# Performance work log

Measured on AMD Instinct MI355X. Metric: run time of the kernel, lower is better.

## Reference

```python
import jax, jax.numpy as jnp
import numpy as np

VOCAB, D, L, H, B, S = 10000, 512, 6, 8, 32, 384
DK = D // H
DFF = 4 * D
EPS = 1e-5


def setup_inputs() -> dict:
    key = jax.random.key(0)
    ks = jax.random.split(key, 24)
    sc = 0.02
    emb = jax.random.normal(ks[0], (VOCAB, D), jnp.float32) * sc
    emb = emb.at[0].set(0.0)  # padding_idx=0
    inp = {
        'input_id': jax.random.randint(ks[1], (B, S), 0, VOCAB),
        'intensity': jax.random.uniform(ks[2], (B, 1, S), jnp.float32),
        'emb': emb,
        'iw': jax.random.normal(ks[3], (1, D), jnp.float32) * sc,
        'ib': jnp.zeros((D,), jnp.float32),
        'Wq': jax.random.normal(ks[4], (L, D, D), jnp.float32) * sc,
        'bq': jnp.zeros((L, D), jnp.float32),
        'Wk': jax.random.normal(ks[5], (L, D, D), jnp.float32) * sc,
        'bk': jnp.zeros((L, D), jnp.float32),
        'Wv': jax.random.normal(ks[6], (L, D, D), jnp.float32) * sc,
        'bv': jnp.zeros((L, D), jnp.float32),
        'Wo': jax.random.normal(ks[7], (L, D, D), jnp.float32) * sc,
        'bo': jnp.zeros((L, D), jnp.float32),
        'ln1w': jnp.ones((L, D), jnp.float32),
        'ln1b': jnp.zeros((L, D), jnp.float32),
        'ln2w': jnp.ones((L, D), jnp.float32),
        'ln2b': jnp.zeros((L, D), jnp.float32),
        'W1': jax.random.normal(ks[8], (L, D, DFF), jnp.float32) * sc,
        'b1': jnp.zeros((L, DFF), jnp.float32),
        'W2': jax.random.normal(ks[9], (L, DFF, D), jnp.float32) * sc,
        'b2': jnp.zeros((L, D), jnp.float32),
    }
    return inp


def _ln(x, w, b):
    m = jnp.mean(x, axis=-1, keepdims=True)
    v = jnp.mean((x - m) ** 2, axis=-1, keepdims=True)
    return (x - m) / jnp.sqrt(v + EPS) * w + b


def _block(x, pad_mask, Wq, bq, Wk, bk, Wv, bv, Wo, bo, ln1w, ln1b, ln2w, ln2b, W1, b1, W2, b2):
    b, s, d = x.shape
    h = _ln(x, ln1w, ln1b)
    q = (h @ Wq + bq).reshape(b, s, H, DK).transpose(0, 2, 1, 3)  # [B,H,S,DK]
    k = (h @ Wk + bk).reshape(b, s, H, DK).transpose(0, 2, 1, 3)
    v = (h @ Wv + bv).reshape(b, s, H, DK).transpose(0, 2, 1, 3)
    scores = jnp.einsum('bhqd,bhkd->bhqk', q, k) / jnp.sqrt(jnp.float32(DK))
    scores = jnp.where(pad_mask, -1e9, scores)  # mask keys at pad positions
    p = jax.nn.softmax(scores, axis=-1)
    attn = jnp.einsum('bhqk,bhkd->bhqd', p, v)
    attn = attn.transpose(0, 2, 1, 3).reshape(b, s, d)
    x = x + (attn @ Wo + bo)
    h2 = _ln(x, ln2w, ln2b)
    ffn = jax.nn.gelu(h2 @ W1 + b1, approximate=False) @ W2 + b2
    return x + ffn


def reference(input_id, intensity, emb, iw, ib, Wq, bq, Wk, bk, Wv, bv, Wo, bo,
              ln1w, ln1b, ln2w, ln2b, W1, b1, W2, b2):
    # predict() path of MSBERT (deterministic; training forward adds random masking)
    inten = jnp.swapaxes(intensity, 1, 2) @ iw + ib          # [B,S,D]
    x = emb[input_id] + inten                                 # token emb + intensity proj
    pad_mask = (input_id == 0)[:, None, None, :]              # [B,1,1,S] broadcast over queries
    for i in range(L):
        x = _block(x, pad_mask, Wq[i], bq[i], Wk[i], bk[i], Wv[i], bv[i], Wo[i], bo[i],
                   ln1w[i], ln1b[i], ln2w[i], ln2b[i], W1[i], b1[i], W2[i], b2[i])
    pool = jnp.matmul(intensity, x) / jnp.float32(intensity.shape[1])  # [B,1,D]
    return pool
```

## Files before the change

### kernel.cpp

```cpp
#include <hip/hip_runtime.h>
#include <math.h>

#define VOCAB 10000
#define D 512
#define L 6
#define H 8
#define B 32
#define S 384
#define DK 64
#define DFF 2048
#define TOK (B * S)
#define TD ((size_t)TOK * D)

typedef unsigned short u16;
using bf16x8 = __attribute__((ext_vector_type(8))) short;
using f32x4  = __attribute__((ext_vector_type(4))) float;
using u16x4  = __attribute__((ext_vector_type(4))) unsigned short;

__device__ u16   g_x[TD];
__device__ u16   g_h[TD];
__device__ u16   g_q[TD];
__device__ u16   g_k[TD];
__device__ u16   g_vt[TD];
__device__ u16   g_ffn[(size_t)TOK * DFF];
__device__ u16   g_qkvT[(size_t)L * 3 * D * D];
__device__ u16   g_woT[(size_t)L * D * D];
__device__ u16   g_w1T[(size_t)L * DFF * D];
__device__ u16   g_w2T[(size_t)L * D * DFF];
__device__ float g_bqkv[L * 3 * D];
__device__ float g_pool[B * 6 * D];

__device__ __forceinline__ u16 f2bf(float f) {
  unsigned int u = __builtin_bit_cast(unsigned int, f);
  u = (u + 0x7fffu + ((u >> 16) & 1u)) >> 16;
  return (u16)u;
}
__device__ __forceinline__ float bf2f(u16 v) {
  unsigned int u = ((unsigned int)v) << 16;
  return __builtin_bit_cast(float, u);
}

__device__ __forceinline__ void gld16(const void* g, void* l) {
  __builtin_amdgcn_global_load_lds(
      (const __attribute__((address_space(1))) unsigned int*)g,
      (__attribute__((address_space(3))) unsigned int*)l, 16, 0, 0);
}

__global__ __launch_bounds__(256) void embed_kernel(
    const int* __restrict__ ids, const float* __restrict__ inten,
    const float* __restrict__ emb, const float* __restrict__ iw,
    const float* __restrict__ ib, u16* __restrict__ x) {
  int tok = blockIdx.x;
  int t = threadIdx.x;
  int id = ids[tok];
  float it = inten[tok];
  const float* er = emb + (size_t)id * D;
  u16* xr = x + (size_t)tok * D;
  xr[t]       = f2bf(er[t] + it * iw[t] + ib[t]);
  xr[t + 256] = f2bf(er[t + 256] + it * iw[t + 256] + ib[t + 256]);
}

__global__ __launch_bounds__(256) void ln_kernel(
    const u16* __restrict__ x, const float* __restrict__ w,
    const float* __restrict__ b, u16* __restrict__ out) {
  int tok = blockIdx.x * 4 + (threadIdx.x >> 6);
  int lane = threadIdx.x & 63;
  const u16* xr = x + (size_t)tok * D + lane * 8;
  bf16x8 v8 = *(const bf16x8*)xr;
  float v[8];
  float s = 0.f, ss = 0.f;
  #pragma unroll
  for (int i = 0; i < 8; ++i) {
    v[i] = bf2f((u16)v8[i]);
    s += v[i];
    ss += v[i] * v[i];
  }
  #pragma unroll
  for (int o = 1; o < 64; o <<= 1) {
    s += __shfl_xor(s, o);
    ss += __shfl_xor(ss, o);
  }
  float mean = s * (1.0f / (float)D);
  float var = ss * (1.0f / (float)D) - mean * mean;
  float rstd = rsqrtf(var + 1e-5f);
  float4 w0 = *(const float4*)(w + lane * 8);
  float4 w1 = *(const float4*)(w + lane * 8 + 4);
  float4 b0 = *(const float4*)(b + lane * 8);
  float4 b1 = *(const float4*)(b + lane * 8 + 4);
  float wv[8] = {w0.x, w0.y, w0.z, w0.w, w1.x, w1.y, w1.z, w1.w};
  float bv[8] = {b0.x, b0.y, b0.z, b0.w, b1.x, b1.y, b1.z, b1.w};
  bf16x8 o8;
  #pragma unroll
  for (int i = 0; i < 8; ++i)
    o8[i] = (short)f2bf((v[i] - mean) * rstd * wv[i] + bv[i]);
  *(bf16x8*)(out + (size_t)tok * D + lane * 8) = o8;
}

__global__ __launch_bounds__(256) void transpose_cvt(
    const float* __restrict__ src, u16* __restrict__ dst,
    int K, int N, size_t sstride, size_t dstride) {
  __shared__ float tile[32][33];
  int n0 = blockIdx.x * 32, k0 = blockIdx.y * 32, l = blockIdx.z;
  src += (size_t)l * sstride;
  dst += (size_t)l * dstride;
  int tx = threadIdx.x & 31, ty = threadIdx.x >> 5;
  #pragma unroll
  for (int i = 0; i < 32; i += 8)
    tile[ty + i][tx] = src[(size_t)(k0 + ty + i) * N + n0 + tx];
  __syncthreads();
  #pragma unroll
  for (int i = 0; i < 32; i += 8)
    dst[(size_t)(n0 + ty + i) * K + k0 + tx] = f2bf(tile[tx][ty + i]);
}

__global__ __launch_bounds__(256) void transpose_qkvo(
    const float* __restrict__ Wq, const float* __restrict__ Wk,
    const float* __restrict__ Wv, const float* __restrict__ Wo,
    u16* __restrict__ qkvT, u16* __restrict__ woT) {
  __shared__ float tile[32][33];
  int z = blockIdx.z;
  int l = z >> 2, which = z & 3;
  const float* src = (which == 0 ? Wq : which == 1 ? Wk : which == 2 ? Wv : Wo)
                     + (size_t)l * D * D;
  u16* dst = (which < 3) ? (qkvT + (size_t)l * 3 * D * D + (size_t)which * D * D)
                         : (woT + (size_t)l * D * D);
  int n0 = blockIdx.x * 32, k0 = blockIdx.y * 32;
  int tx = threadIdx.x & 31, ty = threadIdx.x >> 5;
  #pragma unroll
  for (int i = 0; i < 32; i += 8)
    tile[ty + i][tx] = src[(size_t)(k0 + ty + i) * D + n0 + tx];
  __syncthreads();
  #pragma unroll
  for (int i = 0; i < 32; i += 8)
    dst[(size_t)(n0 + ty + i) * D + k0 + tx] = f2bf(tile[tx][ty + i]);
}

__global__ __launch_bounds__(256) void concat_bias(
    const float* __restrict__ bq, const float* __restrict__ bk,
    const float* __restrict__ bv, float* __restrict__ dst) {
  int i = blockIdx.x * 256 + threadIdx.x;
  int l = i / 1536, c = i % 1536;
  float v = (c < 512) ? bq[l * 512 + c]
          : (c < 1024) ? bk[l * 512 + c - 512]
                       : bv[l * 512 + c - 1024];
  dst[i] = v;
}

template <int EPI>
__global__ __launch_bounds__(256) void mfma_gemm(
    const u16* __restrict__ A, const u16* __restrict__ Bt,
    const float* __restrict__ bias,
    u16* __restrict__ Oq, u16* __restrict__ Ok, u16* __restrict__ Ovt,
    int M, int N, int K) {
  __shared__ u16 As[2][128 * 32];
  __shared__ u16 Bs[2][128 * 32];
  int t = threadIdx.x;
  int lane = t & 63, w = t >> 6;
  int wr = w >> 1, wc = w & 1;

  int gm = gridDim.y, gn = gridDim.x;
  int wgid = blockIdx.y * gn + blockIdx.x;
  int xcd = wgid & 7;
  int c = wgid >> 3;
  int rpx = gm >> 3;
  int cg = c / gn;
  int bm = (xcd * rpx + cg) * 128;
  int bn = (c - cg * gn) * 128;

  int l15 = lane & 15, l4 = lane >> 4;

  int gswu = ((t & 3) ^ ((t >> 3) & 3)) * 8;
  const u16* a0 = A + (size_t)(bm + (t >> 2)) * K + gswu;
  const u16* a1 = A + (size_t)(bm + 64 + (t >> 2)) * K + gswu;
  const u16* b0 = Bt + (size_t)(bn + (t >> 2)) * K + gswu;
  const u16* b1 = Bt + (size_t)(bn + 64 + (t >> 2)) * K + gswu;
  unsigned off0 = (unsigned)(t & 192) * 16u;
  unsigned off1 = off0 + 256u * 16u;
  int rxu = (l4 ^ ((l15 >> 1) & 3)) * 8;

  f32x4 acc[4][4];
  #pragma unroll
  for (int mi = 0; mi < 4; ++mi)
    #pragma unroll
    for (int nj = 0; nj < 4; ++nj)
      acc[mi][nj] = f32x4{0.f, 0.f, 0.f, 0.f};

  int nt = K >> 5;

#define STAGE_T(ti, bi) do { int k0s = (ti) * 32;            \
    gld16(a0 + k0s, (char*)As[bi] + off0);                   \
    gld16(a1 + k0s, (char*)As[bi] + off1);                   \
    gld16(b0 + k0s, (char*)Bs[bi] + off0);                   \
    gld16(b1 + k0s, (char*)Bs[bi] + off1); } while (0)

  STAGE_T(0, 0);
  STAGE_T(1, 1);

  for (int tt = 0; tt < nt; ++tt) {
    if (tt < nt - 1) asm volatile("s_waitcnt vmcnt(4)" ::: "memory");
    else             asm volatile("s_waitcnt vmcnt(0)" ::: "memory");
    __builtin_amdgcn_s_barrier();
    __builtin_amdgcn_sched_barrier(0);
    const u16* Asb = As[tt & 1];
    const u16* Bsb = Bs[tt & 1];
    bf16x8 af[4], bfr[4];
    #pragma unroll
    for (int mi = 0; mi < 4; ++mi)
      af[mi] = *(const bf16x8*)(Asb + (wr * 64 + mi * 16 + l15) * 32 + rxu);
    #pragma unroll
    for (int nj = 0; nj < 4; ++nj)
      bfr[nj] = *(const bf16x8*)(Bsb + (wc * 64 + nj * 16 + l15) * 32 + rxu);
    #pragma unroll
    for (int mi = 0; mi < 4; ++mi)
      #pragma unroll
      for (int nj = 0; nj < 4; ++nj)
        acc[mi][nj] = __builtin_amdgcn_mfma_f32_16x16x32_bf16(af[mi], bfr[nj], acc[mi][nj], 0, 0, 0);
    __builtin_amdgcn_sched_barrier(0);
    __builtin_amdgcn_s_barrier();
    if (tt + 2 < nt) STAGE_T(tt + 2, tt & 1);
  }
#undef STAGE_T

  int row00 = bm + wr * 64, col0 = bn + wc * 64;
  #pragma unroll
  for (int mi = 0; mi < 4; ++mi) {
    int rowb = row00 + mi * 16 + l4 * 4;
    #pragma unroll
    for (int nj = 0; nj < 4; ++nj) {
      int col = col0 + nj * 16 + l15;
      float bcol = bias[col];
      if (EPI == 0) {
        if (col < 512) {
          #pragma unroll
          for (int r = 0; r < 4; ++r)
            Oq[(size_t)(rowb + r) * D + col] = f2bf(acc[mi][nj][r] + bcol);
        } else if (col < 1024) {
          #pragma unroll
          for (int r = 0; r < 4; ++r)
            Ok[(size_t)(rowb + r) * D + (col - 512)] = f2bf(acc[mi][nj][r] + bcol);
        } else {
          int cv = col - 1024;
          int hh = cv >> 6, dk = cv & 63;
          int bb = rowb / S, ss = rowb - bb * S;
          u16x4 pk;
          #pragma unroll
          for (int r = 0; r < 4; ++r) pk[r] = f2bf(acc[mi][nj][r] + bcol);
          *(u16x4*)(Ovt + ((size_t)(bb * H + hh) * DK + dk) * S + ss) = pk;
        }
      } else {
        #pragma unroll
        for (int r = 0; r < 4; ++r) {
          float v = acc[mi][nj][r] + bcol;
          v = 0.5f * v * (1.0f + erff(v * 0.70710678118654752f));
          Oq[(size_t)(rowb + r) * N + col] = f2bf(v);
        }
      }
    }
  }
}

__global__ __launch_bounds__(256) void gemm64(
    const u16* __restrict__ A, const u16* __restrict__ Bt,
    const float* __restrict__ bias, u16* __restrict__ Cres,
    int M, int N, int K) {
  __shared__ u16 As[2][64 * 32];
  __shared__ u16 Bs[2][128 * 32];
  int t = threadIdx.x;
  int lane = t & 63, w = t >> 6;
  int wr = w >> 1, wc = w & 1;

  int gm = gridDim.y, gn = gridDim.x;
  int wgid = blockIdx.y * gn + blockIdx.x;
  int xcd = wgid & 7;
  int c = wgid >> 3;
  int rpx = gm >> 3;
  int cg = c / gn;
  int bm = (xcd * rpx + cg) * 64;
  int bn = (c - cg * gn) * 128;

  int l15 = lane & 15, l4 = lane >> 4;

  int arow = t >> 2, ag = t & 3;
  int aswu = (ag ^ ((arow >> 1) & 3)) * 8;
  const u16* a0 = A + (size_t)(bm + arow) * K + aswu;
  const u16* b0 = Bt + (size_t)(bn + arow) * K + aswu;
  const u16* b1 = Bt + (size_t)(bn + 64 + arow) * K + aswu;
  unsigned offA  = (unsigned)(w * 1024);
  unsigned offB0 = (unsigned)(w * 1024);
  unsigned offB1 = offB0 + 4096u;
  int rxu = (l4 ^ ((l15 >> 1) & 3)) * 8;

  f32x4 acc[2][4];
  #pragma unroll
  for (int mi = 0; mi < 2; ++mi)
    #pragma unroll
    for (int nj = 0; nj < 4; ++nj)
      acc[mi][nj] = f32x4{0.f, 0.f, 0.f, 0.f};

  int nt = K >> 5;

#define STG64(ti, bi) do { int k0s = (ti) * 32;              \
    gld16(a0 + k0s, (char*)As[bi] + offA);                   \
    gld16(b0 + k0s, (char*)Bs[bi] + offB0);                  \
    gld16(b1 + k0s, (char*)Bs[bi] + offB1); } while (0)

  STG64(0, 0);
  STG64(1, 1);

  for (int tt = 0; tt < nt; ++tt) {
    if (tt < nt - 1) asm volatile("s_waitcnt vmcnt(3)" ::: "memory");
    else             asm volatile("s_waitcnt vmcnt(0)" ::: "memory");
    __builtin_amdgcn_s_barrier();
    __builtin_amdgcn_sched_barrier(0);
    const u16* Asb = As[tt & 1];
    const u16* Bsb = Bs[tt & 1];
    bf16x8 af[2], bfr[4];
    #pragma unroll
    for (int mi = 0; mi < 2; ++mi)
      af[mi] = *(const bf16x8*)(Asb + (wr * 32 + mi * 16 + l15) * 32 + rxu);
    #pragma unroll
    for (int nj = 0; nj < 4; ++nj)
      bfr[nj] = *(const bf16x8*)(Bsb + (wc * 64 + nj * 16 + l15) * 32 + rxu);
    #pragma unroll
    for (int mi = 0; mi < 2; ++mi)
      #pragma unroll
      for (int nj = 0; nj < 4; ++nj)
        acc[mi][nj] = __builtin_amdgcn_mfma_f32_16x16x32_bf16(af[mi], bfr[nj], acc[mi][nj], 0, 0, 0);
    __builtin_amdgcn_sched_barrier(0);
    __builtin_amdgcn_s_barrier();
    if (tt + 2 < nt) STG64(tt + 2, tt & 1);
  }
#undef STG64

  int row00 = bm + wr * 32, col0 = bn + wc * 64;
  #pragma unroll
  for (int mi = 0; mi < 2; ++mi) {
    int rowb = row00 + mi * 16 + l4 * 4;
    #pragma unroll
    for (int nj = 0; nj < 4; ++nj) {
      int col = col0 + nj * 16 + l15;
      float bcol = bias[col];
      #pragma unroll
      for (int r = 0; r < 4; ++r) {
        size_t ci = (size_t)(rowb + r) * N + col;
        Cres[ci] = f2bf(bf2f(Cres[ci]) + acc[mi][nj][r] + bcol);
      }
    }
  }
}

__global__ __launch_bounds__(256) void attn_mfma(
    const u16* __restrict__ q, const u16* __restrict__ k,
    const u16* __restrict__ vt, const int* __restrict__ ids,
    u16* __restrict__ out) {
  __shared__ u16 Ks[64][72];
  __shared__ u16 Vs[64][72];
  __shared__ u16 Ps[4][32][72];
  __shared__ float Msall[S];
  int t = threadIdx.x, lane = t & 63, w = t >> 6;
  int l15 = lane & 15, l4 = lane >> 4;
  int bh = blockIdx.x;
  int b = bh >> 3, hh = bh & 7;
  int q0 = blockIdx.y * 128 + w * 32;

  for (int i = t; i < S; i += 256)
    Msall[i] = (ids[b * S + i] == 0) ? -1e9f : 0.0f;

  bf16x8 qf[2][2];
  const u16* qbase = q + (size_t)(b * S + q0) * D + hh * DK;
  #pragma unroll
  for (int mi = 0; mi < 2; ++mi)
    #pragma unroll
    for (int ks = 0; ks < 2; ++ks)
      qf[mi][ks] = *(const bf16x8*)(qbase + (size_t)(mi * 16 + l15) * D + ks * 32 + l4 * 8);

  int rr0 = t >> 3, ch0 = t & 7;
  int rr1 = (256 + t) >> 3, ch1 = t & 7;
  const size_t kbase = (size_t)(b * S) * D + hh * DK;
  const size_t vbase = (size_t)(b * H + hh) * DK * S;

  bf16x8 kr0, kr1, vr0, vr1;
  kr0 = *(const bf16x8*)(k + kbase + (size_t)rr0 * D + ch0 * 8);
  kr1 = *(const bf16x8*)(k + kbase + (size_t)rr1 * D + ch1 * 8);
  vr0 = *(const bf16x8*)(vt + vbase + (size_t)rr0 * S + 0 + ch0 * 8);
  vr1 = *(const bf16x8*)(vt + vbase + (size_t)rr1 * S + 0 + ch1 * 8);
  *(bf16x8*)(&Ks[rr0][ch0 * 8]) = kr0;
  *(bf16x8*)(&Ks[rr1][ch1 * 8]) = kr1;
  *(bf16x8*)(&Vs[rr0][ch0 * 8]) = vr0;
  *(bf16x8*)(&Vs[rr1][ch1 * 8]) = vr1;
  __syncthreads();

  float m[8], lsum[8];
  f32x4 accO[2][4];
  #pragma unroll
  for (int i = 0; i < 8; ++i) { m[i] = -3e38f; lsum[i] = 0.f; }
  #pragma unroll
  for (int mi = 0; mi < 2; ++mi)
    #pragma unroll
    for (int nj = 0; nj < 4; ++nj)
      accO[mi][nj] = f32x4{0.f, 0.f, 0.f, 0.f};

  for (int kb = 0; kb < S; kb += 64) {
    bool more = (kb + 64) < S;
    if (more) {
      kr0 = *(const bf16x8*)(k + kbase + (size_t)(kb + 64 + rr0) * D + ch0 * 8);
      kr1 = *(const bf16x8*)(k + kbase + (size_t)(kb + 64 + rr1) * D + ch1 * 8);
      vr0 = *(const bf16x8*)(vt + vbase + (size_t)rr0 * S + kb + 64 + ch0 * 8);
      vr1 = *(const bf16x8*)(vt + vbase + (size_t)rr1 * S + kb + 64 + ch1 * 8);
    }

    f32x4 sc[2][4];
    #pragma unroll
    for (int mi = 0; mi < 2; ++mi)
      #pragma unroll
      for (int nj = 0; nj < 4; ++nj)
        sc[mi][nj] = f32x4{0.f, 0.f, 0.f, 0.f};
    __builtin_amdgcn_s_setprio(1);
    #pragma unroll
    for (int ks = 0; ks < 2; ++ks) {
      bf16x8 kf[4];
      #pragma unroll
      for (int nj = 0; nj < 4; ++nj)
        kf[nj] = *(const bf16x8*)(&Ks[nj * 16 + l15][ks * 32 + l4 * 8]);
      #pragma unroll
      for (int mi = 0; mi < 2; ++mi)
        #pragma unroll
        for (int nj = 0; nj < 4; ++nj)
          sc[mi][nj] = __builtin_amdgcn_mfma_f32_16x16x32_bf16(qf[mi][ks], kf[nj], sc[mi][nj], 0, 0, 0);
    }
    __builtin_amdgcn_s_setprio(0);
    #pragma unroll
    for (int mi = 0; mi < 2; ++mi)
      #pragma unroll
      for (int nj = 0; nj < 4; ++nj) {
        float mv = Msall[kb + nj * 16 + l15];
        #pragma unroll
        for (int r = 0; r < 4; ++r)
          sc[mi][nj][r] = sc[mi][nj][r] * 0.125f + mv;
      }
    #pragma unroll
    for (int mi = 0; mi < 2; ++mi)
      #pragma unroll
      for (int r = 0; r < 4; ++r) {
        int ridx = mi * 4 + r;
        float mx = sc[mi][0][r];
        #pragma unroll
        for (int nj = 1; nj < 4; ++nj) mx = fmaxf(mx, sc[mi][nj][r]);
        #pragma unroll
        for (int o = 1; o < 16; o <<= 1) mx = fmaxf(mx, __shfl_xor(mx, o));
        float mnew = fmaxf(m[ridx], mx);
        float scale = __expf(m[ridx] - mnew);
        float rs = 0.f;
        #pragma unroll
        for (int nj = 0; nj < 4; ++nj) {
          float p = __expf(sc[mi][nj][r] - mnew);
          sc[mi][nj][r] = p;
          rs += p;
        }
        #pragma unroll
        for (int o = 1; o < 16; o <<= 1) rs += __shfl_xor(rs, o);
        lsum[ridx] = lsum[ridx] * scale + rs;
        m[ridx] = mnew;
        #pragma unroll
        for (int nj = 0; nj < 4; ++nj) accO[mi][nj][r] *= scale;
      }
    #pragma unroll
    for (int mi = 0; mi < 2; ++mi)
      #pragma unroll
      for (int nj = 0; nj < 4; ++nj)
        #pragma unroll
        for (int r = 0; r < 4; ++r)
          Ps[w][mi * 16 + l4 * 4 + r][nj * 16 + l15] = f2bf(sc[mi][nj][r]);
    __builtin_amdgcn_s_setprio(1);
    #pragma unroll
    for (int ks2 = 0; ks2 < 2; ++ks2) {
      bf16x8 pf[2], vf[4];
      #pragma unroll
      for (int mi = 0; mi < 2; ++mi)
        pf[mi] = *(const bf16x8*)(&Ps[w][mi * 16 + l15][ks2 * 32 + l4 * 8]);
      #pragma unroll
      for (int nj = 0; nj < 4; ++nj)
        vf[nj] = *(const bf16x8*)(&Vs[nj * 16 + l15][ks2 * 32 + l4 * 8]);
      #pragma unroll
      for (int mi = 0; mi < 2; ++mi)
        #pragma unroll
        for (int nj = 0; nj < 4; ++nj)
          accO[mi][nj] = __builtin_amdgcn_mfma_f32_16x16x32_bf16(pf[mi], vf[nj], accO[mi][nj], 0, 0, 0);
    }
    __builtin_amdgcn_s_setprio(0);

    if (more) {
      __syncthreads();
      *(bf16x8*)(&Ks[rr0][ch0 * 8]) = kr0;
      *(bf16x8*)(&Ks[rr1][ch1 * 8]) = kr1;
      *(bf16x8*)(&Vs[rr0][ch0 * 8]) = vr0;
      *(bf16x8*)(&Vs[rr1][ch1 * 8]) = vr1;
      __syncthreads();
    }
  }

  #pragma unroll
  for (int mi = 0; mi < 2; ++mi)
    #pragma unroll
    for (int nj = 0; nj < 4; ++nj)
      #pragma unroll
      for (int r = 0; r < 4; ++r) {
        int row = b * S + q0 + mi * 16 + l4 * 4 + r;
        out[(size_t)row * D + hh * DK + nj * 16 + l15] =
            f2bf(accO[mi][nj][r] / lsum[mi * 4 + r]);
      }
}

__global__ __launch_bounds__(512) void pool_part(
    const u16* __restrict__ x, const float* __restrict__ inten,
    float* __restrict__ part) {
  int b = blockIdx.x, cchunk = blockIdx.y;
  int d = threadIdx.x;
  int s0 = cchunk * 64;
  float acc = 0.f;
  for (int s = s0; s < s0 + 64; ++s)
    acc += inten[b * S + s] * bf2f(x[((size_t)b * S + s) * D + d]);
  part[((size_t)b * 6 + cchunk) * D + d] = acc;
}
__global__ __launch_bounds__(512) void pool_reduce(
    const float* __restrict__ part, float* __restrict__ out) {
  int b = blockIdx.x, d = threadIdx.x;
  float acc = 0.f;
  #pragma unroll
  for (int c = 0; c < 6; ++c) acc += part[((size_t)b * 6 + c) * D + d];
  out[b * D + d] = acc;
}

extern "C" void kernel_launch(void* const* d_in, const int* in_sizes, int n_in,
                              void* d_out, int out_size, void* d_ws, size_t ws_size,
                              hipStream_t stream) {
  const int* input_id    = (const int*)d_in[0];
  const float* intensity = (const float*)d_in[1];
  const float* emb = (const float*)d_in[2];
  const float* iw  = (const float*)d_in[3];
  const float* ib  = (const float*)d_in[4];
  const float* Wq  = (const float*)d_in[5];
  const float* bq  = (const float*)d_in[6];
  const float* Wk  = (const float*)d_in[7];
  const float* bk  = (const float*)d_in[8];
  const float* Wv  = (const float*)d_in[9];
  const float* bv  = (const float*)d_in[10];
  const float* Wo  = (const float*)d_in[11];
  const float* bo  = (const float*)d_in[12];
  const float* ln1w = (const float*)d_in[13];
  const float* ln1b = (const float*)d_in[14];
  const float* ln2w = (const float*)d_in[15];
  const float* ln2b = (const float*)d_in[16];
  const float* W1  = (const float*)d_in[17];
  const float* b1  = (const float*)d_in[18];
  const float* W2  = (const float*)d_in[19];
  const float* b2  = (const float*)d_in[20];
  float* outp = (float*)d_out;

  float *bqkv, *poolp;
  u16 *x, *h, *q, *k, *vt, *ffn, *qkvT, *woT, *w1T, *w2T;
  { void* p; hipGetSymbolAddress(&p, HIP_SYMBOL(g_x));    x    = (u16*)p; }
  { void* p; hipGetSymbolAddress(&p, HIP_SYMBOL(g_h));    h    = (u16*)p; }
  { void* p; hipGetSymbolAddress(&p, HIP_SYMBOL(g_q));    q    = (u16*)p; }
  { void* p; hipGetSymbolAddress(&p, HIP_SYMBOL(g_k));    k    = (u16*)p; }
  { void* p; hipGetSymbolAddress(&p, HIP_SYMBOL(g_vt));   vt   = (u16*)p; }
  { void* p; hipGetSymbolAddress(&p, HIP_SYMBOL(g_ffn));  ffn  = (u16*)p; }
  { void* p; hipGetSymbolAddress(&p, HIP_SYMBOL(g_qkvT)); qkvT = (u16*)p; }
  { void* p; hipGetSymbolAddress(&p, HIP_SYMBOL(g_woT));  woT  = (u16*)p; }
  { void* p; hipGetSymbolAddress(&p, HIP_SYMBOL(g_w1T));  w1T  = (u16*)p; }
  { void* p; hipGetSymbolAddress(&p, HIP_SYMBOL(g_w2T));  w2T  = (u16*)p; }
  { void* p; hipGetSymbolAddress(&p, HIP_SYMBOL(g_bqkv)); bqkv = (float*)p; }
  { void* p; hipGetSymbolAddress(&p, HIP_SYMBOL(g_pool)); poolp = (float*)p; }

  dim3 t256(256);
  transpose_qkvo<<<dim3(16, 16, 4 * L), t256, 0, stream>>>(Wq, Wk, Wv, Wo, qkvT, woT);
  transpose_cvt<<<dim3(64, 16, L), t256, 0, stream>>>(W1, w1T, D, DFF, (size_t)D * DFF, (size_t)D * DFF);
  transpose_cvt<<<dim3(16, 64, L), t256, 0, stream>>>(W2, w2T, DFF, D, (size_t)DFF * D, (size_t)DFF * D);
  concat_bias<<<L * 3 * D / 256, t256, 0, stream>>>(bq, bk, bv, bqkv);

  embed_kernel<<<TOK, t256, 0, stream>>>(input_id, intensity, emb, iw, ib, x);

  for (int l = 0; l < L; ++l) {
    const u16* qkvT_l = qkvT + (size_t)l * 3 * D * D;
    const u16* woT_l  = woT + (size_t)l * D * D;
    const u16* w1T_l  = w1T + (size_t)l * D * DFF;
    const u16* w2T_l  = w2T + (size_t)l * DFF * D;

    ln_kernel<<<TOK / 4, t256, 0, stream>>>(x, ln1w + (size_t)l * D, ln1b + (size_t)l * D, h);
    mfma_gemm<0><<<dim3(12, 96), t256, 0, stream>>>(h, qkvT_l, bqkv + l * 3 * D,
                                                    q, k, vt, TOK, 3 * D, D);
    attn_mfma<<<dim3(B * H, S / 128), t256, 0, stream>>>(q, k, vt, input_id, h);
    gemm64<<<dim3(4, 192), t256, 0, stream>>>(h, woT_l, bo + (size_t)l * D,
                                              x, TOK, D, D);
    ln_kernel<<<TOK / 4, t256, 0, stream>>>(x, ln2w + (size_t)l * D, ln2b + (size_t)l * D, h);
    mfma_gemm<2><<<dim3(16, 96), t256, 0, stream>>>(h, w1T_l, b1 + (size_t)l * DFF,
                                                    ffn, nullptr, nullptr, TOK, DFF, D);
    gemm64<<<dim3(4, 192), t256, 0, stream>>>(ffn, w2T_l, b2 + (size_t)l * D,
                                              x, TOK, D, DFF);
  }

  pool_part<<<dim3(B, 6), dim3(512), 0, stream>>>(x, intensity, poolp);
  pool_reduce<<<B, dim3(512), 0, stream>>>(poolp, outp);
}
```

Before: 1.240 ms.

## Prepack weights into MFMA fragment layout and load B directly to registers

Weights are now converted once into a fragment-major bf16 layout that matches the MFMA B operand, so each wave can load its B fragments from global memory straight into registers instead of staging them through LDS. This cuts LDS traffic and LDS footprint in both GEMM kernels, keeps a two-deep register double buffer for B, and adjusts the vmcnt waits to match. Block order is also remapped so that consecutive workgroups on an XCD walk M first within the same N column, which should improve L2 reuse of B. The cost is more vector registers per thread and global B loads duplicated across the two row-waves, which now go through cache instead of shared memory.

```diff
diff --git a/kernel.cpp b/kernel.cpp
--- a/kernel.cpp
+++ b/kernel.cpp
@@ -23,10 +23,10 @@
 __device__ u16   g_k[TD];
 __device__ u16   g_vt[TD];
 __device__ u16   g_ffn[(size_t)TOK * DFF];
-__device__ u16   g_qkvT[(size_t)L * 3 * D * D];
-__device__ u16   g_woT[(size_t)L * D * D];
-__device__ u16   g_w1T[(size_t)L * DFF * D];
-__device__ u16   g_w2T[(size_t)L * D * DFF];
+__device__ u16   g_qkvB[(size_t)L * 3 * D * D];
+__device__ u16   g_woB[(size_t)L * D * D];
+__device__ u16   g_w1B[(size_t)L * DFF * D];
+__device__ u16   g_w2B[(size_t)L * D * DFF];
 __device__ float g_bqkv[L * 3 * D];
 __device__ float g_pool[B * 6 * D];
 
@@ -96,43 +96,23 @@
   *(bf16x8*)(out + (size_t)tok * D + lane * 8) = o8;
 }
 
-__global__ __launch_bounds__(256) void transpose_cvt(
-    const float* __restrict__ src, u16* __restrict__ dst,
-    int K, int N, size_t sstride, size_t dstride) {
-  __shared__ float tile[32][33];
-  int n0 = blockIdx.x * 32, k0 = blockIdx.y * 32, l = blockIdx.z;
-  src += (size_t)l * sstride;
-  dst += (size_t)l * dstride;
-  int tx = threadIdx.x & 31, ty = threadIdx.x >> 5;
-  #pragma unroll
-  for (int i = 0; i < 32; i += 8)
-    tile[ty + i][tx] = src[(size_t)(k0 + ty + i) * N + n0 + tx];
-  __syncthreads();
-  #pragma unroll
-  for (int i = 0; i < 32; i += 8)
-    dst[(size_t)(n0 + ty + i) * K + k0 + tx] = f2bf(tile[tx][ty + i]);
-}
-
-__global__ __launch_bounds__(256) void transpose_qkvo(
-    const float* __restrict__ Wq, const float* __restrict__ Wk,
-    const float* __restrict__ Wv, const float* __restrict__ Wo,
-    u16* __restrict__ qkvT, u16* __restrict__ woT) {
-  __shared__ float tile[32][33];
-  int z = blockIdx.z;
-  int l = z >> 2, which = z & 3;
-  const float* src = (which == 0 ? Wq : which == 1 ? Wk : which == 2 ? Wv : Wo)
-                     + (size_t)l * D * D;
-  u16* dst = (which < 3) ? (qkvT + (size_t)l * 3 * D * D + (size_t)which * D * D)
-                         : (woT + (size_t)l * D * D);
-  int n0 = blockIdx.x * 32, k0 = blockIdx.y * 32;
-  int tx = threadIdx.x & 31, ty = threadIdx.x >> 5;
-  #pragma unroll
-  for (int i = 0; i < 32; i += 8)
-    tile[ty + i][tx] = src[(size_t)(k0 + ty + i) * D + n0 + tx];
-  __syncthreads();
-  #pragma unroll
-  for (int i = 0; i < 32; i += 8)
-    dst[(size_t)(n0 + ty + i) * D + k0 + tx] = f2bf(tile[tx][ty + i]);
+__global__ __launch_bounds__(256) void prepack_b(
+    const float* __restrict__ W, u16* __restrict__ Bp,
+    int N, int K, size_t sstride, size_t dstride) {
+  int l = blockIdx.y;
+  W += (size_t)l * sstride;
+  Bp += (size_t)l * dstride;
+  int fi = blockIdx.x * 4 + (threadIdx.x >> 6);
+  int lane = threadIdx.x & 63;
+  int nfr = K >> 5;
+  int nb = fi / nfr, kb = fi - nb * nfr;
+  int col = nb * 16 + (lane & 15);
+  int row0 = kb * 32 + (lane >> 4) * 8;
+  bf16x8 o;
+  #pragma unroll
+  for (int j = 0; j < 8; ++j)
+    o[j] = (short)f2bf(W[(size_t)(row0 + j) * N + col]);
+  *(bf16x8*)(Bp + (size_t)fi * 512 + lane * 8) = o;
 }
 
 __global__ __launch_bounds__(256) void concat_bias(
@@ -148,36 +128,33 @@
 
 template <int EPI>
 __global__ __launch_bounds__(256) void mfma_gemm(
-    const u16* __restrict__ A, const u16* __restrict__ Bt,
+    const u16* __restrict__ A, const u16* __restrict__ Bp,
     const float* __restrict__ bias,
     u16* __restrict__ Oq, u16* __restrict__ Ok, u16* __restrict__ Ovt,
     int M, int N, int K) {
   __shared__ u16 As[2][128 * 32];
-  __shared__ u16 Bs[2][128 * 32];
   int t = threadIdx.x;
   int lane = t & 63, w = t >> 6;
   int wr = w >> 1, wc = w & 1;
+  int l15 = lane & 15, l4 = lane >> 4;
 
   int gm = gridDim.y, gn = gridDim.x;
   int wgid = blockIdx.y * gn + blockIdx.x;
-  int xcd = wgid & 7;
-  int c = wgid >> 3;
-  int rpx = gm >> 3;
-  int cg = c / gn;
-  int bm = (xcd * rpx + cg) * 128;
-  int bn = (c - cg * gn) * 128;
-
-  int l15 = lane & 15, l4 = lane >> 4;
+  int xcd = wgid & 7, c = wgid >> 3, rpx = gm >> 3;
+  int bni = c / rpx;
+  int bm = (xcd * rpx + (c - bni * rpx)) * 128;
+  int bn = bni * 128;
 
   int gswu = ((t & 3) ^ ((t >> 3) & 3)) * 8;
   const u16* a0 = A + (size_t)(bm + (t >> 2)) * K + gswu;
   const u16* a1 = A + (size_t)(bm + 64 + (t >> 2)) * K + gswu;
-  const u16* b0 = Bt + (size_t)(bn + (t >> 2)) * K + gswu;
-  const u16* b1 = Bt + (size_t)(bn + 64 + (t >> 2)) * K + gswu;
   unsigned off0 = (unsigned)(t & 192) * 16u;
   unsigned off1 = off0 + 256u * 16u;
   int rxu = (l4 ^ ((l15 >> 1) & 3)) * 8;
 
+  int nfr = K >> 5;
+  const u16* bpw = Bp + ((size_t)((bn >> 4) + wc * 4) * nfr) * 512 + lane * 8;
+
   f32x4 acc[4][4];
   #pragma unroll
   for (int mi = 0; mi < 4; ++mi)
@@ -185,41 +162,43 @@
     for (int nj = 0; nj < 4; ++nj)
       acc[mi][nj] = f32x4{0.f, 0.f, 0.f, 0.f};
 
-  int nt = K >> 5;
-
-#define STAGE_T(ti, bi) do { int k0s = (ti) * 32;            \
+  int nt = nfr;
+
+#define STAGE_A(ti, bi) do { int k0s = (ti) * 32;            \
     gld16(a0 + k0s, (char*)As[bi] + off0);                   \
-    gld16(a1 + k0s, (char*)As[bi] + off1);                   \
-    gld16(b0 + k0s, (char*)Bs[bi] + off0);                   \
-    gld16(b1 + k0s, (char*)Bs[bi] + off1); } while (0)
-
-  STAGE_T(0, 0);
-  STAGE_T(1, 1);
-
-  for (int tt = 0; tt < nt; ++tt) {
-    if (tt < nt - 1) asm volatile("s_waitcnt vmcnt(4)" ::: "memory");
-    else             asm volatile("s_waitcnt vmcnt(0)" ::: "memory");
-    __builtin_amdgcn_s_barrier();
-    __builtin_amdgcn_sched_barrier(0);
-    const u16* Asb = As[tt & 1];
-    const u16* Bsb = Bs[tt & 1];
-    bf16x8 af[4], bfr[4];
-    #pragma unroll
-    for (int mi = 0; mi < 4; ++mi)
-      af[mi] = *(const bf16x8*)(Asb + (wr * 64 + mi * 16 + l15) * 32 + rxu);
-    #pragma unroll
-    for (int nj = 0; nj < 4; ++nj)
-      bfr[nj] = *(const bf16x8*)(Bsb + (wc * 64 + nj * 16 + l15) * 32 + rxu);
-    #pragma unroll
-    for (int mi = 0; mi < 4; ++mi)
-      #pragma unroll
-      for (int nj = 0; nj < 4; ++nj)
-        acc[mi][nj] = __builtin_amdgcn_mfma_f32_16x16x32_bf16(af[mi], bfr[nj], acc[mi][nj], 0, 0, 0);
-    __builtin_amdgcn_sched_barrier(0);
-    __builtin_amdgcn_s_barrier();
-    if (tt + 2 < nt) STAGE_T(tt + 2, tt & 1);
-  }
-#undef STAGE_T
+    gld16(a1 + k0s, (char*)As[bi] + off1); } while (0)
+#define LOADB(ti, breg) do {                                 \
+    _Pragma("unroll") for (int nj = 0; nj < 4; ++nj)         \
+      breg[nj] = *(const bf16x8*)(bpw + ((size_t)nj * nfr + (ti)) * 512); } while (0)
+
+  bf16x8 brA[4], brB[4];
+  STAGE_A(0, 0); LOADB(0, brA);
+  STAGE_A(1, 1); LOADB(1, brB);
+
+#define GSTEP(tt, breg) do {                                             \
+    if ((tt) < nt - 1) asm volatile("s_waitcnt vmcnt(6)" ::: "memory");  \
+    else               asm volatile("s_waitcnt vmcnt(0)" ::: "memory");  \
+    __builtin_amdgcn_s_barrier();                                        \
+    __builtin_amdgcn_sched_barrier(0);                                   \
+    const u16* Asb = As[(tt) & 1];                                       \
+    bf16x8 af[4];                                                        \
+    _Pragma("unroll") for (int mi = 0; mi < 4; ++mi)                     \
+      af[mi] = *(const bf16x8*)(Asb + (wr * 64 + mi * 16 + l15) * 32 + rxu); \
+    _Pragma("unroll") for (int mi = 0; mi < 4; ++mi)                     \
+      _Pragma("unroll") for (int nj = 0; nj < 4; ++nj)                   \
+        acc[mi][nj] = __builtin_amdgcn_mfma_f32_16x16x32_bf16(af[mi], breg[nj], acc[mi][nj], 0, 0, 0); \
+    __builtin_amdgcn_sched_barrier(0);                                   \
+    __builtin_amdgcn_s_barrier();                                        \
+    if ((tt) + 2 < nt) { STAGE_A((tt) + 2, (tt) & 1); LOADB((tt) + 2, breg); } \
+  } while (0)
+
+  for (int tt = 0; tt < nt; tt += 2) {
+    GSTEP(tt, brA);
+    GSTEP(tt + 1, brB);
+  }
+#undef GSTEP
+#undef LOADB
+#undef STAGE_A
 
   int row00 = bm + wr * 64, col0 = bn + wc * 64;
   #pragma unroll
@@ -260,35 +239,31 @@
 }
 
 __global__ __launch_bounds__(256) void gemm64(
-    const u16* __restrict__ A, const u16* __restrict__ Bt,
+    const u16* __restrict__ A, const u16* __restrict__ Bp,
     const float* __restrict__ bias, u16* __restrict__ Cres,
     int M, int N, int K) {
   __shared__ u16 As[2][64 * 32];
-  __shared__ u16 Bs[2][128 * 32];
   int t = threadIdx.x;
   int lane = t & 63, w = t >> 6;
   int wr = w >> 1, wc = w & 1;
 
   int gm = gridDim.y, gn = gridDim.x;
   int wgid = blockIdx.y * gn + blockIdx.x;
-  int xcd = wgid & 7;
-  int c = wgid >> 3;
-  int rpx = gm >> 3;
-  int cg = c / gn;
-  int bm = (xcd * rpx + cg) * 64;
-  int bn = (c - cg * gn) * 128;
+  int xcd = wgid & 7, c = wgid >> 3, rpx = gm >> 3;
+  int bni = c / rpx;
+  int bm = (xcd * rpx + (c - bni * rpx)) * 64;
+  int bn = bni * 128;
 
   int l15 = lane & 15, l4 = lane >> 4;
 
   int arow = t >> 2, ag = t & 3;
   int aswu = (ag ^ ((arow >> 1) & 3)) * 8;
   const u16* a0 = A + (size_t)(bm + arow) * K + aswu;
-  const u16* b0 = Bt + (size_t)(bn + arow) * K + aswu;
-  const u16* b1 = Bt + (size_t)(bn + 64 + arow) * K + aswu;
-  unsigned offA  = (unsigned)(w * 1024);
-  unsigned offB0 = (unsigned)(w * 1024);
-  unsigned offB1 = offB0 + 4096u;
+  unsigned offA = (unsigned)(w * 1024);
   int rxu = (l4 ^ ((l15 >> 1) & 3)) * 8;
+
+  int nfr = K >> 5;
+  const u16* bpw = Bp + ((size_t)((bn >> 4) + wc * 4) * nfr) * 512 + lane * 8;
 
   f32x4 acc[2][4];
   #pragma unroll
@@ -297,40 +272,42 @@
     for (int nj = 0; nj < 4; ++nj)
       acc[mi][nj] = f32x4{0.f, 0.f, 0.f, 0.f};
 
-  int nt = K >> 5;
-
-#define STG64(ti, bi) do { int k0s = (ti) * 32;              \
-    gld16(a0 + k0s, (char*)As[bi] + offA);                   \
-    gld16(b0 + k0s, (char*)Bs[bi] + offB0);                  \
-    gld16(b1 + k0s, (char*)Bs[bi] + offB1); } while (0)
-
-  STG64(0, 0);
-  STG64(1, 1);
-
-  for (int tt = 0; tt < nt; ++tt) {
-    if (tt < nt - 1) asm volatile("s_waitcnt vmcnt(3)" ::: "memory");
-    else             asm volatile("s_waitcnt vmcnt(0)" ::: "memory");
-    __builtin_amdgcn_s_barrier();
-    __builtin_amdgcn_sched_barrier(0);
-    const u16* Asb = As[tt & 1];
-    const u16* Bsb = Bs[tt & 1];
-    bf16x8 af[2], bfr[4];
-    #pragma unroll
-    for (int mi = 0; mi < 2; ++mi)
-      af[mi] = *(const bf16x8*)(Asb + (wr * 32 + mi * 16 + l15) * 32 + rxu);
-    #pragma unroll
-    for (int nj = 0; nj < 4; ++nj)
-      bfr[nj] = *(const bf16x8*)(Bsb + (wc * 64 + nj * 16 + l15) * 32 + rxu);
-    #pragma unroll
-    for (int mi = 0; mi < 2; ++mi)
-      #pragma unroll
-      for (int nj = 0; nj < 4; ++nj)
-        acc[mi][nj] = __builtin_amdgcn_mfma_f32_16x16x32_bf16(af[mi], bfr[nj], acc[mi][nj], 0, 0, 0);
-    __builtin_amdgcn_sched_barrier(0);
-    __builtin_amdgcn_s_barrier();
-    if (tt + 2 < nt) STG64(tt + 2, tt & 1);
-  }
-#undef STG64
+  int nt = nfr;
+
+#define STAGE_A(ti, bi) \
+    gld16(a0 + (ti) * 32, (char*)As[bi] + offA)
+#define LOADB(ti, breg) do {                                 \
+    _Pragma("unroll") for (int nj = 0; nj < 4; ++nj)         \
+      breg[nj] = *(const bf16x8*)(bpw + ((size_t)nj * nfr + (ti)) * 512); } while (0)
+
+  bf16x8 brA[4], brB[4];
+  STAGE_A(0, 0); LOADB(0, brA);
+  STAGE_A(1, 1); LOADB(1, brB);
+
+#define GSTEP(tt, breg) do {                                             \
+    if ((tt) < nt - 1) asm volatile("s_waitcnt vmcnt(5)" ::: "memory");  \
+    else               asm volatile("s_waitcnt vmcnt(0)" ::: "memory");  \
+    __builtin_amdgcn_s_barrier();                                        \
+    __builtin_amdgcn_sched_barrier(0);                                   \
+    const u16* Asb = As[(tt) & 1];                                       \
+    bf16x8 af[2];                                                        \
+    _Pragma("unroll") for (int mi = 0; mi < 2; ++mi)                     \
+      af[mi] = *(const bf16x8*)(Asb + (wr * 32 + mi * 16 + l15) * 32 + rxu); \
+    _Pragma("unroll") for (int mi = 0; mi < 2; ++mi)                     \
+      _Pragma("unroll") for (int nj = 0; nj < 4; ++nj)                   \
+        acc[mi][nj] = __builtin_amdgcn_mfma_f32_16x16x32_bf16(af[mi], breg[nj], acc[mi][nj], 0, 0, 0); \
+    __builtin_amdgcn_sched_barrier(0);                                   \
+    __builtin_amdgcn_s_barrier();                                        \
+    if ((tt) + 2 < nt) { STAGE_A((tt) + 2, (tt) & 1); LOADB((tt) + 2, breg); } \
+  } while (0)
+
+  for (int tt = 0; tt < nt; tt += 2) {
+    GSTEP(tt, brA);
+    GSTEP(tt + 1, brB);
+  }
+#undef GSTEP
+#undef LOADB
+#undef STAGE_A
 
   int row00 = bm + wr * 32, col0 = bn + wc * 64;
   #pragma unroll
@@ -558,44 +535,47 @@
   float* outp = (float*)d_out;
 
   float *bqkv, *poolp;
-  u16 *x, *h, *q, *k, *vt, *ffn, *qkvT, *woT, *w1T, *w2T;
+  u16 *x, *h, *q, *k, *vt, *ffn, *qkvB, *woB, *w1B, *w2B;
   { void* p; hipGetSymbolAddress(&p, HIP_SYMBOL(g_x));    x    = (u16*)p; }
   { void* p; hipGetSymbolAddress(&p, HIP_SYMBOL(g_h));    h    = (u16*)p; }
   { void* p; hipGetSymbolAddress(&p, HIP_SYMBOL(g_q));    q    = (u16*)p; }
   { void* p; hipGetSymbolAddress(&p, HIP_SYMBOL(g_k));    k    = (u16*)p; }
   { void* p; hipGetSymbolAddress(&p, HIP_SYMBOL(g_vt));   vt   = (u16*)p; }
   { void* p; hipGetSymbolAddress(&p, HIP_SYMBOL(g_ffn));  ffn  = (u16*)p; }
-  { void* p; hipGetSymbolAddress(&p, HIP_SYMBOL(g_qkvT)); qkvT = (u16*)p; }
-  { void* p; hipGetSymbolAddress(&p, HIP_SYMBOL(g_woT));  woT  = (u16*)p; }
-  { void* p; hipGetSymbolAddress(&p, HIP_SYMBOL(g_w1T));  w1T  = (u16*)p; }
-  { void* p; hipGetSymbolAddress(&p, HIP_SYMBOL(g_w2T));  w2T  = (u16*)p; }
+  { void* p; hipGetSymbolAddress(&p, HIP_SYMBOL(g_qkvB)); qkvB = (u16*)p; }
+  { void* p; hipGetSymbolAddress(&p, HIP_SYMBOL(g_woB));  woB  = (u16*)p; }
+  { void* p; hipGetSymbolAddress(&p, HIP_SYMBOL(g_w1B));  w1B  = (u16*)p; }
+  { void* p; hipGetSymbolAddress(&p, HIP_SYMBOL(g_w2B));  w2B  = (u16*)p; }
   { void* p; hipGetSymbolAddress(&p, HIP_SYMBOL(g_bqkv)); bqkv = (float*)p; }
   { void* p; hipGetSymbolAddress(&p, HIP_SYMBOL(g_pool)); poolp = (float*)p; }
 
   dim3 t256(256);
-  transpose_qkvo<<<dim3(16, 16, 4 * L), t256, 0, stream>>>(Wq, Wk, Wv, Wo, qkvT, woT);
-  transpose_cvt<<<dim3(64, 16, L), t256, 0, stream>>>(W1, w1T, D, DFF, (size_t)D * DFF, (size_t)D * DFF);
-  transpose_cvt<<<dim3(16, 64, L), t256, 0, stream>>>(W2, w2T, DFF, D, (size_t)DFF * D, (size_t)DFF * D);
+  prepack_b<<<dim3(128, L), t256, 0, stream>>>(Wq, qkvB + 0 * D * D, D, D, (size_t)D * D, (size_t)3 * D * D);
+  prepack_b<<<dim3(128, L), t256, 0, stream>>>(Wk, qkvB + 1 * D * D, D, D, (size_t)D * D, (size_t)3 * D * D);
+  prepack_b<<<dim3(128, L), t256, 0, stream>>>(Wv, qkvB + 2 * D * D, D, D, (size_t)D * D, (size_t)3 * D * D);
+  prepack_b<<<dim3(128, L), t256, 0, stream>>>(Wo, woB, D, D, (size_t)D * D, (size_t)D * D);
+  prepack_b<<<dim3(512, L), t256, 0, stream>>>(W1, w1B, DFF, D, (size_t)D * DFF, (size_t)DFF * D);
+  prepack_b<<<dim3(512, L), t256, 0, stream>>>(W2, w2B, D, DFF, (size_t)DFF * D, (size_t)D * DFF);
   concat_bias<<<L * 3 * D / 256, t256, 0, stream>>>(bq, bk, bv, bqkv);
 
   embed_kernel<<<TOK, t256, 0, stream>>>(input_id, intensity, emb, iw, ib, x);
 
   for (int l = 0; l < L; ++l) {
-    const u16* qkvT_l = qkvT + (size_t)l * 3 * D * D;
-    const u16* woT_l  = woT + (size_t)l * D * D;
-    const u16* w1T_l  = w1T + (size_t)l * D * DFF;
-    const u16* w2T_l  = w2T + (size_t)l * DFF * D;
+    const u16* qkvB_l = qkvB + (size_t)l * 3 * D * D;
+    const u16* woB_l  = woB + (size_t)l * D * D;
+    const u16* w1B_l  = w1B + (size_t)l * DFF * D;
+    const u16* w2B_l  = w2B + (size_t)l * D * DFF;
 
     ln_kernel<<<TOK / 4, t256, 0, stream>>>(x, ln1w + (size_t)l * D, ln1b + (size_t)l * D, h);
-    mfma_gemm<0><<<dim3(12, 96), t256, 0, stream>>>(h, qkvT_l, bqkv + l * 3 * D,
+    mfma_gemm<0><<<dim3(12, 96), t256, 0, stream>>>(h, qkvB_l, bqkv + l * 3 * D,
                                                     q, k, vt, TOK, 3 * D, D);
     attn_mfma<<<dim3(B * H, S / 128), t256, 0, stream>>>(q, k, vt, input_id, h);
-    gemm64<<<dim3(4, 192), t256, 0, stream>>>(h, woT_l, bo + (size_t)l * D,
+    gemm64<<<dim3(4, 192), t256, 0, stream>>>(h, woB_l, bo + (size_t)l * D,
                                               x, TOK, D, D);
     ln_kernel<<<TOK / 4, t256, 0, stream>>>(x, ln2w + (size_t)l * D, ln2b + (size_t)l * D, h);
-    mfma_gemm<2><<<dim3(16, 96), t256, 0, stream>>>(h, w1T_l, b1 + (size_t)l * DFF,
+    mfma_gemm<2><<<dim3(16, 96), t256, 0, stream>>>(h, w1B_l, b1 + (size_t)l * DFF,
                                                     ffn, nullptr, nullptr, TOK, DFF, D);
-    gemm64<<<dim3(4, 192), t256, 0, stream>>>(ffn, w2T_l, b2 + (size_t)l * D,
+    gemm64<<<dim3(4, 192), t256, 0, stream>>>(ffn, w2B_l, b2 + (size_t)l * D,
                                               x, TOK, D, DFF);
   }
 
```

New measurement: 1.360 ms. +9.7%, slower.
